# Kernel optimization log

Measured on AMD Instinct MI355X. Metric: run time of the kernel, lower is better.

## Reference

```python
import jax, jax.numpy as jnp
import numpy as np

D_MODEL = 1024
N_HEADS = 16
HEAD_DIM = D_MODEL // N_HEADS
D_FF = 4096
ROPE_RANK = 16
LN_EPS = 1e-5


def _ln(x, g, b):
    mu = jnp.mean(x, axis=-1, keepdims=True)
    var = jnp.mean((x - mu) ** 2, axis=-1, keepdims=True)
    return (x - mu) * jax.lax.rsqrt(var + LN_EPS) * g + b


def _rope(x, A, B_):
    # x: [B, T, D]; learned low-rank additive correction to sin/cos tables
    B, T, D = x.shape
    pos = jnp.arange(T, dtype=jnp.float32)
    theta = 1.0 / (10000.0 ** (jnp.arange(0, D, 2, dtype=jnp.float32) / D))  # [D/2]
    angles = pos[:, None] * theta[None, :]                                   # [T, D/2]
    sin_pos, cos_pos = jnp.sin(angles), jnp.cos(angles)
    base = jnp.concatenate([sin_pos, cos_pos], axis=-1)                      # [T, D]
    learned = (base @ A) @ B_                                                # [T, D]
    l_sin, l_cos = jnp.split(learned, 2, axis=-1)
    sin_f = sin_pos + l_sin                                                  # [T, D/2]
    cos_f = cos_pos + l_cos
    xe, xo = x[..., ::2], x[..., 1::2]
    re = xe * cos_f[None] - xo * sin_f[None]
    ro = xe * sin_f[None] + xo * cos_f[None]
    return jnp.stack([re, ro], axis=-1).reshape(B, T, D)


def setup_inputs() -> dict:
    key = jax.random.key(0)
    ks = jax.random.split(key, 20)
    B, T = 2, 2048
    s = 1.0 / np.sqrt(D_MODEL)
    sf = 1.0 / np.sqrt(D_FF)
    sr = 1.0 / np.sqrt(ROPE_RANK)
    return {
        "tgt": jax.random.normal(ks[0], (B, T, D_MODEL), jnp.float32),
        "Wq": jax.random.normal(ks[1], (D_MODEL, D_MODEL), jnp.float32) * s,
        "bq": jnp.zeros((D_MODEL,), jnp.float32),
        "Wk": jax.random.normal(ks[2], (D_MODEL, D_MODEL), jnp.float32) * s,
        "bk": jnp.zeros((D_MODEL,), jnp.float32),
        "Wv": jax.random.normal(ks[3], (D_MODEL, D_MODEL), jnp.float32) * s,
        "bv": jnp.zeros((D_MODEL,), jnp.float32),
        "Wo": jax.random.normal(ks[4], (D_MODEL, D_MODEL), jnp.float32) * s,
        "bo": jnp.zeros((D_MODEL,), jnp.float32),
        "W1": jax.random.normal(ks[5], (D_MODEL, D_FF), jnp.float32) * s,
        "b1": jnp.zeros((D_FF,), jnp.float32),
        "W2": jax.random.normal(ks[6], (D_FF, D_MODEL), jnp.float32) * sf,
        "b2": jnp.zeros((D_MODEL,), jnp.float32),
        "ln1_g": jnp.ones((D_MODEL,), jnp.float32),
        "ln1_b": jnp.zeros((D_MODEL,), jnp.float32),
        "ln2_g": jnp.ones((D_MODEL,), jnp.float32),
        "ln2_b": jnp.zeros((D_MODEL,), jnp.float32),
        "rope_A": jax.random.normal(ks[7], (D_MODEL, ROPE_RANK), jnp.float32) * s,
        "rope_B": jax.random.normal(ks[8], (ROPE_RANK, D_MODEL), jnp.float32) * sr,
    }


def reference(tgt, Wq, bq, Wk, bk, Wv, bv, Wo, bo, W1, b1, W2, b2,
              ln1_g, ln1_b, ln2_g, ln2_b, rope_A, rope_B):
    x = tgt
    B, T, D = x.shape
    q = _rope(x @ Wq + bq, rope_A, rope_B)
    k = _rope(x @ Wk + bk, rope_A, rope_B)
    v = x @ Wv + bv
    # [B, H, T, hd]
    q = q.reshape(B, T, N_HEADS, HEAD_DIM).transpose(0, 2, 1, 3)
    k = k.reshape(B, T, N_HEADS, HEAD_DIM).transpose(0, 2, 1, 3)
    v = v.reshape(B, T, N_HEADS, HEAD_DIM).transpose(0, 2, 1, 3)
    scores = jnp.einsum("bhqd,bhkd->bhqk", q, k) / np.sqrt(HEAD_DIM)
    attn = jax.nn.softmax(scores, axis=-1)  # no mask: module applies none
    ctx = jnp.einsum("bhqk,bhkd->bhqd", attn, v)
    ctx = ctx.transpose(0, 2, 1, 3).reshape(B, T, D)
    x = x + (ctx @ Wo + bo)
    x = _ln(x, ln1_g, ln1_b)
    ff = jax.nn.relu(x @ W1 + b1) @ W2 + b2
    x = _ln(x + ff, ln2_g, ln2_b)
    return x
```

## Files before the change

### kernel.cpp

```cpp
#include <hip/hip_runtime.h>
#include <math.h>

typedef unsigned short u16;
typedef unsigned int u32;
typedef __attribute__((ext_vector_type(8))) short short8v;
typedef __attribute__((ext_vector_type(4))) float f32x4;

__device__ __forceinline__ u16 f2bf(float f) {
    u32 u = __float_as_uint(f);
    u32 r = (u + 0x7fffu + ((u >> 16) & 1u)) >> 16;
    return (u16)r;
}

#define GLOAD_LDS(g, l)                                                        \
    __builtin_amdgcn_global_load_lds(                                          \
        (const __attribute__((address_space(1))) void*)(g),                    \
        (__attribute__((address_space(3))) void*)(l), 16, 0, 0)

__global__ void cast_k(const float* __restrict__ x, u16* __restrict__ y) {
    const int gid = blockIdx.x * blockDim.x + threadIdx.x;
    float4 v = ((const float4*)x)[gid];
    ushort4 o;
    o.x = f2bf(v.x); o.y = f2bf(v.y); o.z = f2bf(v.z); o.w = f2bf(v.w);
    ((ushort4*)y)[gid] = o;
}

__global__ __launch_bounds__(256) void tcast_k(const float* __restrict__ S,
                                               u16* __restrict__ Dt,
                                               int K, int N) {
    __shared__ float tile[32][33];
    const int n0 = blockIdx.x * 32, k0 = blockIdx.y * 32;
    const int tx = threadIdx.x & 31, ty = threadIdx.x >> 5;
#pragma unroll
    for (int i = 0; i < 4; i++)
        tile[ty + 8 * i][tx] = S[(size_t)(k0 + ty + 8 * i) * N + n0 + tx];
    __syncthreads();
#pragma unroll
    for (int i = 0; i < 4; i++)
        Dt[(size_t)(n0 + ty + 8 * i) * K + k0 + tx] = f2bf(tile[tx][ty + 8 * i]);
}

__global__ __launch_bounds__(256) void vtrans_k(const u16* __restrict__ vv,
                                                u16* __restrict__ Vt) {
    __shared__ u16 tile[32][33];
    const int key0 = blockIdx.x * 32, d0 = blockIdx.y * 32, bh = blockIdx.z;
    const int b = bh >> 4, h = bh & 15;
    const int tx = threadIdx.x & 31, ty = threadIdx.x >> 5;
#pragma unroll
    for (int i = 0; i < 4; i++)
        tile[ty + 8 * i][tx] =
            vv[(size_t)(b * 2048 + key0 + ty + 8 * i) * 1024 + h * 64 + d0 + tx];
    __syncthreads();
#pragma unroll
    for (int i = 0; i < 4; i++) {
        const int d = d0 + ty + 8 * i;
        const int key = key0 + tx;
        const int ksw = (key & ~63) | ((((key >> 3) & 7) ^ (d & 7)) << 3) | (key & 7);
        Vt[((size_t)bh * 64 + d) * 2048 + ksw] = tile[tx][ty + 8 * i];
    }
}

#define ROPE_LOG2C (13.287712379549449f / 512.0f)

__global__ __launch_bounds__(256) void rope1_k(const float* __restrict__ A,
                                               float* __restrict__ P) {
    __shared__ float sc[16][17];
    __shared__ float cc[16][17];
    __shared__ float Als[16][17];
    __shared__ float Alc[16][17];
    const int tid = threadIdx.x;
    const int tt = tid >> 4, rr = tid & 15;
    const int t = blockIdx.x * 16 + tt;
    float acc = 0.f;
    for (int i0 = 0; i0 < 512; i0 += 16) {
        __syncthreads();
        {
            const int i = i0 + rr;
            const float th = exp2f(-(float)i * ROPE_LOG2C);
            const float ang = (float)t * th;
            sc[tt][rr] = sinf(ang);
            cc[tt][rr] = cosf(ang);
            Als[tt][rr] = A[(i0 + tt) * 16 + rr];
            Alc[tt][rr] = A[(512 + i0 + tt) * 16 + rr];
        }
        __syncthreads();
#pragma unroll
        for (int ii = 0; ii < 16; ++ii)
            acc = fmaf(sc[tt][ii], Als[ii][rr],
                       fmaf(cc[tt][ii], Alc[ii][rr], acc));
    }
    P[t * 16 + rr] = acc;
}

__global__ void rope2_k(const float* __restrict__ P, const float* __restrict__ Bw,
                        float* __restrict__ sf, float* __restrict__ cf) {
    const int gid = blockIdx.x * blockDim.x + threadIdx.x;
    if (gid >= 2048 * 512) return;
    const int t = gid >> 9, i = gid & 511;
    float ls = 0.f, lc = 0.f;
#pragma unroll
    for (int r = 0; r < 16; ++r) {
        const float p = P[t * 16 + r];
        ls = fmaf(p, Bw[r * 1024 + i], ls);
        lc = fmaf(p, Bw[r * 1024 + 512 + i], lc);
    }
    const float th = exp2f(-(float)i * ROPE_LOG2C);
    const float ang = (float)t * th;
    sf[gid] = sinf(ang) + ls;
    cf[gid] = cosf(ang) + lc;
}

__device__ __forceinline__ void xcd_tile(int L, int xn, int rn, int rm,
                                         int& tm, int& tn) {
    const int xcd = L & 7, i = L >> 3;
    const int cx = xcd % xn, cy = xcd / xn;
    tn = cx * rn + (i % rn);
    tm = cy * rm + (i / rn);
}

enum { EP_NONE = 0, EP_RES = 2, EP_RELU = 3 };

template <int EPI, bool CBF, int BN>
__global__ __launch_bounds__(256) void mgemm_k(
    const u16* __restrict__ A, const u16* __restrict__ Bt,
    const float* __restrict__ bias, const float* __restrict__ resf,
    void* __restrict__ Cp, int M, int N, int K, int xn, int rn, int rm) {
    constexpr int NT = BN / 32;
    __shared__ u16 As[2 * 128 * 32];
    __shared__ u16 Bs[2 * BN * 32];
    const int tid = threadIdx.x;
    const int w = tid >> 6, l = tid & 63;
    const int quad = l >> 4, lr = l & 15;
    const int wr = w >> 1, wc = w & 1;
    int tm, tn;
    xcd_tile(blockIdx.x, xn, rn, rm, tm, tn);
    const int m0 = tm * 128, n0 = tn * BN;

    const int srow = w * 16 + (l >> 2);
    const int scol = (l & 3) * 8;
    const u16* ag0 = A + (size_t)(m0 + srow) * K + scol;
    const u16* ag1 = A + (size_t)(m0 + 64 + srow) * K + scol;
    const u16* bg0 = Bt + (size_t)(n0 + srow) * K + scol;
    const u16* bg1 = Bt + (size_t)(n0 + 64 + srow) * K + scol;

    f32x4 acc[4][NT];
#pragma unroll
    for (int i = 0; i < 4; i++)
#pragma unroll
        for (int j = 0; j < NT; j++) acc[i][j] = (f32x4)(0.0f);

    {
        u16* Ab = As;
        u16* Bb = Bs;
        GLOAD_LDS(ag0, Ab + w * 512);
        GLOAD_LDS(ag1, Ab + 2048 + w * 512);
        GLOAD_LDS(bg0, Bb + w * 512);
        if (BN == 128) GLOAD_LDS(bg1, Bb + 2048 + w * 512);
    }

    const int niter = K >> 5;
    for (int i = 0; i < niter; ++i) {
        __syncthreads();
        const int knext = (i + 1) << 5;
        if (knext < K) {
            u16* Ab = As + ((i + 1) & 1) * 4096;
            u16* Bb = Bs + ((i + 1) & 1) * (BN * 32);
            GLOAD_LDS(ag0 + knext, Ab + w * 512);
            GLOAD_LDS(ag1 + knext, Ab + 2048 + w * 512);
            GLOAD_LDS(bg0 + knext, Bb + w * 512);
            if (BN == 128) GLOAD_LDS(bg1 + knext, Bb + 2048 + w * 512);
        }
        const u16* Ac = As + (i & 1) * 4096;
        const u16* Bc = Bs + (i & 1) * (BN * 32);
        short8v af[4], bf[NT];
#pragma unroll
        for (int mt = 0; mt < 4; ++mt)
            af[mt] = *(const short8v*)&Ac[(wr * 64 + mt * 16 + lr) * 32 + quad * 8];
#pragma unroll
        for (int nt = 0; nt < NT; ++nt)
            bf[nt] = *(const short8v*)&Bc[(wc * (BN / 2) + nt * 16 + lr) * 32 + quad * 8];
#pragma unroll
        for (int mt = 0; mt < 4; ++mt)
#pragma unroll
            for (int nt = 0; nt < NT; ++nt)
                acc[mt][nt] = __builtin_amdgcn_mfma_f32_16x16x32_bf16(
                    af[mt], bf[nt], acc[mt][nt], 0, 0, 0);
    }

#pragma unroll
    for (int mt = 0; mt < 4; ++mt) {
#pragma unroll
        for (int nt = 0; nt < NT; ++nt) {
            const int n = n0 + wc * (BN / 2) + nt * 16 + lr;
            const float bb = bias[n];
#pragma unroll
            for (int reg = 0; reg < 4; ++reg) {
                const int m = m0 + wr * 64 + mt * 16 + quad * 4 + reg;
                float v = acc[mt][nt][reg] + bb;
                if (EPI == EP_RES) v += resf[(size_t)m * N + n];
                if (EPI == EP_RELU) v = fmaxf(v, 0.f);
                if (CBF) ((u16*)Cp)[(size_t)m * N + n] = f2bf(v);
                else     ((float*)Cp)[(size_t)m * N + n] = v;
            }
        }
    }
}

__global__ __launch_bounds__(256) void mqkv_k(
    const u16* __restrict__ A, const u16* __restrict__ Bt,
    const float* __restrict__ bq, const float* __restrict__ bk,
    const float* __restrict__ bv, const float* __restrict__ sf,
    const float* __restrict__ cf, u16* __restrict__ out) {
    const int K = 1024;
    __shared__ u16 As[2 * 128 * 32];
    __shared__ u16 Bs[2 * 128 * 32];
    const int tid = threadIdx.x;
    const int w = tid >> 6, l = tid & 63;
    const int quad = l >> 4, lr = l & 15;
    const int wr = w >> 1, wc = w & 1;
    int tm, tn;
    xcd_tile(blockIdx.x, 4, 6, 16, tm, tn);
    const int m0 = tm * 128, n0 = tn * 128;

    const int srow = w * 16 + (l >> 2);
    const int scol = (l & 3) * 8;
    const u16* ag0 = A + (size_t)(m0 + srow) * K + scol;
    const u16* ag1 = A + (size_t)(m0 + 64 + srow) * K + scol;
    const u16* bg0 = Bt + (size_t)(n0 + srow) * K + scol;
    const u16* bg1 = Bt + (size_t)(n0 + 64 + srow) * K + scol;

    f32x4 acc[4][4];
#pragma unroll
    for (int i = 0; i < 4; i++)
#pragma unroll
        for (int j = 0; j < 4; j++) acc[i][j] = (f32x4)(0.0f);

    {
        GLOAD_LDS(ag0, As + w * 512);
        GLOAD_LDS(ag1, As + 2048 + w * 512);
        GLOAD_LDS(bg0, Bs + w * 512);
        GLOAD_LDS(bg1, Bs + 2048 + w * 512);
    }
    for (int i = 0; i < 32; ++i) {
        __syncthreads();
        const int knext = (i + 1) << 5;
        if (knext < K) {
            u16* Ab = As + ((i + 1) & 1) * 4096;
            u16* Bb = Bs + ((i + 1) & 1) * 4096;
            GLOAD_LDS(ag0 + knext, Ab + w * 512);
            GLOAD_LDS(ag1 + knext, Ab + 2048 + w * 512);
            GLOAD_LDS(bg0 + knext, Bb + w * 512);
            GLOAD_LDS(bg1 + knext, Bb + 2048 + w * 512);
        }
        const u16* Ac = As + (i & 1) * 4096;
        const u16* Bc = Bs + (i & 1) * 4096;
        short8v af[4], bf[4];
#pragma unroll
        for (int mt = 0; mt < 4; ++mt)
            af[mt] = *(const short8v*)&Ac[(wr * 64 + mt * 16 + lr) * 32 + quad * 8];
#pragma unroll
        for (int nt = 0; nt < 4; ++nt)
            bf[nt] = *(const short8v*)&Bc[(wc * 64 + nt * 16 + lr) * 32 + quad * 8];
#pragma unroll
        for (int mt = 0; mt < 4; ++mt)
#pragma unroll
            for (int nt = 0; nt < 4; ++nt)
                acc[mt][nt] = __builtin_amdgcn_mfma_f32_16x16x32_bf16(
                    af[mt], bf[nt], acc[mt][nt], 0, 0, 0);
    }

    const int which = n0 >> 10;
    const float* bias = which == 0 ? bq : (which == 1 ? bk : bv);
    const bool doRope = which < 2;
    u16* Cp = out + (size_t)which * 4096 * 1024;

#pragma unroll
    for (int mt = 0; mt < 4; ++mt) {
#pragma unroll
        for (int nt = 0; nt < 4; ++nt) {
            const int n = n0 + wc * 64 + nt * 16 + lr;
            const int col = n & 1023;
            const float bb = bias[col];
#pragma unroll
            for (int reg = 0; reg < 4; ++reg) {
                const int m = m0 + wr * 64 + mt * 16 + quad * 4 + reg;
                float v = acc[mt][nt][reg] + bb;
                const float partner = __shfl_xor(v, 1);
                int colw = col;
                if (doRope) {
                    const int t = m & 2047;
                    const int fi = col >> 1;
                    const float svv = sf[t * 512 + fi];
                    const float cvv = cf[t * 512 + fi];
                    v = (col & 1) ? fmaf(partner, svv, v * cvv)
                                  : fmaf(v, cvv, -partner * svv);
                    if (which == 0) v *= 0.125f;
                    colw = (col & ~63) | ((((col >> 3) & 7) ^ (m & 7)) << 3) |
                           (col & 7);
                }
                Cp[(size_t)m * 1024 + colw] = f2bf(v);
            }
        }
    }
}

__global__ __launch_bounds__(256) void mattn_k(
    const u16* __restrict__ Q, const u16* __restrict__ Kg,
    const u16* __restrict__ Vt, u16* __restrict__ O) {
    __shared__ u16 Qs[64 * 64];
    __shared__ u16 Ks[64 * 64];
    __shared__ u16 Vs[64 * 64];
    __shared__ u16 Ps[4][16][72];
    const int tid = threadIdx.x;
    const int w = tid >> 6, l = tid & 63;
    const int quad = l >> 4, lr = l & 15;
    const int L = blockIdx.x;
    const int bh = (L & 7) * 4 + ((L >> 3) & 3);
    const int b = bh >> 4, h = bh & 15;
    const int row0 = (L >> 5) * 64;
    const size_t base = (size_t)b * 2048 * 1024 + (size_t)h * 64;
    const size_t vbase = (size_t)bh * 64 * 2048;

    const int dr = l >> 3;
    const int dc = (l & 7) * 8;
    const int g0 = w * 2, g1 = w * 2 + 1;

    GLOAD_LDS(Q + base + (size_t)(row0 + g0 * 8 + dr) * 1024 + dc, Qs + g0 * 512);
    GLOAD_LDS(Q + base + (size_t)(row0 + g1 * 8 + dr) * 1024 + dc, Qs + g1 * 512);
    __syncthreads();
    const int qr = w * 16 + lr;
    const short8v aq0 = *(const short8v*)&Qs[qr * 64 + ((quad ^ (qr & 7)) << 3)];
    const short8v aq1 = *(const short8v*)&Qs[qr * 64 + (((quad + 4) ^ (qr & 7)) << 3)];

    float lsum[4] = {0.f, 0.f, 0.f, 0.f};
    f32x4 o_acc[4];
#pragma unroll
    for (int nt = 0; nt < 4; nt++) o_acc[nt] = (f32x4)(0.0f);

    for (int kc = 0; kc < 2048; kc += 64) {
        __syncthreads();
        GLOAD_LDS(Kg + base + (size_t)(kc + g0 * 8 + dr) * 1024 + dc, Ks + g0 * 512);
        GLOAD_LDS(Kg + base + (size_t)(kc + g1 * 8 + dr) * 1024 + dc, Ks + g1 * 512);
        GLOAD_LDS(Vt + vbase + (size_t)(g0 * 8 + dr) * 2048 + kc + dc, Vs + g0 * 512);
        GLOAD_LDS(Vt + vbase + (size_t)(g1 * 8 + dr) * 2048 + kc + dc, Vs + g1 * 512);
        __syncthreads();

        f32x4 s[4];
#pragma unroll
        for (int nt = 0; nt < 4; nt++) s[nt] = (f32x4)(0.0f);
#pragma unroll
        for (int nt = 0; nt < 4; nt++) {
            const int kr = nt * 16 + lr;
            short8v bk0 = *(const short8v*)&Ks[kr * 64 + ((quad ^ (kr & 7)) << 3)];
            short8v bk1 = *(const short8v*)&Ks[kr * 64 + (((quad + 4) ^ (kr & 7)) << 3)];
            s[nt] = __builtin_amdgcn_mfma_f32_16x16x32_bf16(aq0, bk0, s[nt], 0, 0, 0);
            s[nt] = __builtin_amdgcn_mfma_f32_16x16x32_bf16(aq1, bk1, s[nt], 0, 0, 0);
        }

#pragma unroll
        for (int nt = 0; nt < 4; nt++) {
#pragma unroll
            for (int reg = 0; reg < 4; reg++) {
                const float p = __expf(s[nt][reg]);
                lsum[reg] += p;
                Ps[w][quad * 4 + reg][nt * 16 + lr] = f2bf(p);
            }
        }
        const short8v ap0 = *(const short8v*)&Ps[w][lr][quad * 8];
        const short8v ap1 = *(const short8v*)&Ps[w][lr][32 + quad * 8];
#pragma unroll
        for (int nt = 0; nt < 4; nt++) {
            const int vr = nt * 16 + lr;
            short8v vf0 = *(const short8v*)&Vs[vr * 64 + ((quad ^ (vr & 7)) << 3)];
            short8v vf1 = *(const short8v*)&Vs[vr * 64 + (((quad + 4) ^ (vr & 7)) << 3)];
            o_acc[nt] = __builtin_amdgcn_mfma_f32_16x16x32_bf16(ap0, vf0, o_acc[nt], 0, 0, 0);
            o_acc[nt] = __builtin_amdgcn_mfma_f32_16x16x32_bf16(ap1, vf1, o_acc[nt], 0, 0, 0);
        }
    }

    float l_i[4];
#pragma unroll
    for (int reg = 0; reg < 4; reg++) {
        float t = lsum[reg];
        t += __shfl_xor(t, 1);
        t += __shfl_xor(t, 2);
        t += __shfl_xor(t, 4);
        t += __shfl_xor(t, 8);
        l_i[reg] = t;
    }

#pragma unroll
    for (int nt = 0; nt < 4; nt++)
#pragma unroll
        for (int reg = 0; reg < 4; reg++) {
            const float out = o_acc[nt][reg] / l_i[reg];
            O[base + (size_t)(row0 + w * 16 + quad * 4 + reg) * 1024 +
              nt * 16 + lr] = f2bf(out);
        }
}

__global__ __launch_bounds__(256) void ln_k(
    const float* __restrict__ X, const float* __restrict__ g,
    const float* __restrict__ bb, float* __restrict__ outf,
    u16* __restrict__ outb) {
    const int row = blockIdx.x, tid = threadIdx.x;
    const float* x = X + (size_t)row * 1024;
    float4 xv = *(const float4*)&x[tid * 4];
    float s = xv.x + xv.y + xv.z + xv.w;
    float s2 = xv.x * xv.x + xv.y * xv.y + xv.z * xv.z + xv.w * xv.w;
#pragma unroll
    for (int msk = 32; msk >= 1; msk >>= 1) {
        s += __shfl_xor(s, msk);
        s2 += __shfl_xor(s2, msk);
    }
    __shared__ float red[8];
    const int wv = tid >> 6;
    if ((tid & 63) == 0) { red[wv] = s; red[wv + 4] = s2; }
    __syncthreads();
    s = red[0] + red[1] + red[2] + red[3];
    s2 = red[4] + red[5] + red[6] + red[7];
    const float mu = s * (1.f / 1024.f);
    float var = s2 * (1.f / 1024.f) - mu * mu;
    var = fmaxf(var, 0.f);
    const float rstd = rsqrtf(var + 1e-5f);
    float4 g4 = *(const float4*)&g[tid * 4];
    float4 b4 = *(const float4*)&bb[tid * 4];
    float o0 = (xv.x - mu) * rstd * g4.x + b4.x;
    float o1 = (xv.y - mu) * rstd * g4.y + b4.y;
    float o2 = (xv.z - mu) * rstd * g4.z + b4.z;
    float o3 = (xv.w - mu) * rstd * g4.w + b4.w;
    if (outf)
        *(float4*)(outf + (size_t)row * 1024 + tid * 4) = make_float4(o0, o1, o2, o3);
    if (outb) {
        ushort4 ov;
        ov.x = f2bf(o0); ov.y = f2bf(o1); ov.z = f2bf(o2); ov.w = f2bf(o3);
        *(ushort4*)(outb + (size_t)row * 1024 + tid * 4) = ov;
    }
}

extern "C" void kernel_launch(void* const* d_in, const int* in_sizes, int n_in,
                              void* d_out, int out_size, void* d_ws, size_t ws_size,
                              hipStream_t stream) {
    const float* tgt = (const float*)d_in[0];
    const float* Wq  = (const float*)d_in[1];
    const float* bq  = (const float*)d_in[2];
    const float* Wk  = (const float*)d_in[3];
    const float* bk  = (const float*)d_in[4];
    const float* Wv  = (const float*)d_in[5];
    const float* bv  = (const float*)d_in[6];
    const float* Wo  = (const float*)d_in[7];
    const float* bo  = (const float*)d_in[8];
    const float* W1  = (const float*)d_in[9];
    const float* b1  = (const float*)d_in[10];
    const float* W2  = (const float*)d_in[11];
    const float* b2  = (const float*)d_in[12];
    const float* g1  = (const float*)d_in[13];
    const float* be1 = (const float*)d_in[14];
    const float* g2  = (const float*)d_in[15];
    const float* be2 = (const float*)d_in[16];
    const float* rA  = (const float*)d_in[17];
    const float* rB  = (const float*)d_in[18];

    const int M = 4096, D = 1024, DFF = 4096;
    const size_t MD = (size_t)M * D;
    const size_t MB = 1u << 20;
    char* wsb = (char*)d_ws;

    u16* q    = (u16*)wsb;
    u16* vv   = q + 2 * MD;
    u16* ctx  = q + 3 * MD;
    u16* h    = q;
    float* x1  = (float*)(wsb + 32 * MB);
    float* sfp = (float*)(wsb + 48 * MB);
    float* cfp = sfp + (size_t)2048 * 512;
    u16* x1b  = (u16*)sfp;
    u16* tgtb = (u16*)(wsb + 56 * MB);
    u16* Vt   = (u16*)(wsb + 56 * MB);
    u16* Wqt  = (u16*)(wsb + 64 * MB);
    u16* Wkt  = (u16*)(wsb + 66 * MB);
    u16* Wvt  = (u16*)(wsb + 68 * MB);
    u16* Wot  = (u16*)(wsb + 70 * MB);
    u16* W1t  = (u16*)(wsb + 72 * MB);
    u16* W2t  = (u16*)(wsb + 80 * MB);
    float* Pp = (float*)(wsb + 88 * MB);

    cast_k<<<dim3(4096), dim3(256), 0, stream>>>(tgt, tgtb);
    tcast_k<<<dim3(32, 32),  dim3(256), 0, stream>>>(Wq, Wqt, D, D);
    tcast_k<<<dim3(32, 32),  dim3(256), 0, stream>>>(Wk, Wkt, D, D);
    tcast_k<<<dim3(32, 32),  dim3(256), 0, stream>>>(Wv, Wvt, D, D);
    tcast_k<<<dim3(32, 32),  dim3(256), 0, stream>>>(Wo, Wot, D, D);
    tcast_k<<<dim3(128, 32), dim3(256), 0, stream>>>(W1, W1t, D, DFF);
    tcast_k<<<dim3(32, 128), dim3(256), 0, stream>>>(W2, W2t, DFF, D);
    rope1_k<<<dim3(128), dim3(256), 0, stream>>>(rA, Pp);
    rope2_k<<<dim3(4096), dim3(256), 0, stream>>>(Pp, rB, sfp, cfp);

    mqkv_k<<<dim3(768), dim3(256), 0, stream>>>(
        tgtb, Wqt, bq, bk, bv, sfp, cfp, q);

    vtrans_k<<<dim3(64, 2, 32), dim3(256), 0, stream>>>(vv, Vt);

    mattn_k<<<dim3(1024), dim3(256), 0, stream>>>(q, q + MD, Vt, ctx);

    mgemm_k<EP_RES, false, 64><<<dim3(512), dim3(256), 0, stream>>>(
        ctx, Wot, bo, tgt, x1, M, D, D, 2, 8, 8);
    ln_k<<<dim3(4096), dim3(256), 0, stream>>>(x1, g1, be1, x1, x1b);
    mgemm_k<EP_RELU, true, 128><<<dim3(1024), dim3(256), 0, stream>>>(
        x1b, W1t, b1, nullptr, h, M, DFF, D, 4, 8, 16);
    mgemm_k<EP_RES, false, 64><<<dim3(512), dim3(256), 0, stream>>>(
        h, W2t, b2, x1, x1, M, D, DFF, 2, 8, 8);
    ln_k<<<dim3(4096), dim3(256), 0, stream>>>(x1, g2, be2, (float*)d_out, nullptr);

    (void)in_sizes; (void)n_in; (void)out_size; (void)ws_size;
}
```

Measured before the change: 471.8 us.

## Double-buffer K/V and widen attention tile to 128 query rows

Rewrites the attention kernel so each block handles 128 query rows (32 per wave), halving the grid and reusing each K/V tile across twice as many queries. K/V tiles are double-buffered so the next tile's global-to-LDS load overlaps the current compute, and one barrier per iteration replaces two. QK^T is computed transposed (K as A operand) so P can be written back into the Q LDS buffer with packed bf16 conversion, and launch bounds request 3 blocks per CU. The risk is higher register pressure from doubled accumulators and fewer blocks (512) to fill the GPU.

```diff
diff --git a/kernel.cpp b/kernel.cpp
--- a/kernel.cpp
+++ b/kernel.cpp
@@ -304,99 +304,159 @@
     }
 }
 
-__global__ __launch_bounds__(256) void mattn_k(
+__global__ __launch_bounds__(256, 3) void mattn_k(
     const u16* __restrict__ Q, const u16* __restrict__ Kg,
     const u16* __restrict__ Vt, u16* __restrict__ O) {
-    __shared__ u16 Qs[64 * 64];
-    __shared__ u16 Ks[64 * 64];
-    __shared__ u16 Vs[64 * 64];
-    __shared__ u16 Ps[4][16][72];
+    __shared__ u16 QPs[128 * 64];
+    __shared__ u16 Ks[2][64 * 64];
+    __shared__ u16 Vs[2][64 * 64];
     const int tid = threadIdx.x;
     const int w = tid >> 6, l = tid & 63;
     const int quad = l >> 4, lr = l & 15;
     const int L = blockIdx.x;
     const int bh = (L & 7) * 4 + ((L >> 3) & 3);
     const int b = bh >> 4, h = bh & 15;
-    const int row0 = (L >> 5) * 64;
+    const int row0 = (L >> 5) * 128;
     const size_t base = (size_t)b * 2048 * 1024 + (size_t)h * 64;
     const size_t vbase = (size_t)bh * 64 * 2048;
 
     const int dr = l >> 3;
     const int dc = (l & 7) * 8;
-    const int g0 = w * 2, g1 = w * 2 + 1;
-
-    GLOAD_LDS(Q + base + (size_t)(row0 + g0 * 8 + dr) * 1024 + dc, Qs + g0 * 512);
-    GLOAD_LDS(Q + base + (size_t)(row0 + g1 * 8 + dr) * 1024 + dc, Qs + g1 * 512);
+    const int g0 = w * 2, g1 = g0 + 1;
+    const u16* kg0 = Kg + base + (size_t)(g0 * 8 + dr) * 1024 + dc;
+    const u16* kg1 = Kg + base + (size_t)(g1 * 8 + dr) * 1024 + dc;
+    const u16* vg0 = Vt + vbase + (size_t)(g0 * 8 + dr) * 2048 + dc;
+    const u16* vg1 = Vt + vbase + (size_t)(g1 * 8 + dr) * 2048 + dc;
+
+#pragma unroll
+    for (int j = 0; j < 4; ++j) {
+        const int g = w * 4 + j;
+        GLOAD_LDS(Q + base + (size_t)(row0 + g * 8 + dr) * 1024 + dc,
+                  QPs + g * 512);
+    }
+    GLOAD_LDS(kg0, Ks[0] + g0 * 512);
+    GLOAD_LDS(kg1, Ks[0] + g1 * 512);
+    GLOAD_LDS(vg0, Vs[0] + g0 * 512);
+    GLOAD_LDS(vg1, Vs[0] + g1 * 512);
     __syncthreads();
-    const int qr = w * 16 + lr;
-    const short8v aq0 = *(const short8v*)&Qs[qr * 64 + ((quad ^ (qr & 7)) << 3)];
-    const short8v aq1 = *(const short8v*)&Qs[qr * 64 + (((quad + 4) ^ (qr & 7)) << 3)];
-
-    float lsum[4] = {0.f, 0.f, 0.f, 0.f};
-    f32x4 o_acc[4];
-#pragma unroll
-    for (int nt = 0; nt < 4; nt++) o_acc[nt] = (f32x4)(0.0f);
-
-    for (int kc = 0; kc < 2048; kc += 64) {
+
+    const int rsw = lr & 7;
+    short8v qf[2][2];
+#pragma unroll
+    for (int ntq = 0; ntq < 2; ++ntq) {
+        const int qr = w * 32 + ntq * 16 + lr;
+#pragma unroll
+        for (int kh = 0; kh < 2; ++kh)
+            qf[ntq][kh] = *(const short8v*)&QPs[qr * 64 +
+                (((kh * 4 + quad) ^ rsw) << 3)];
+    }
+
+    f32x4 o_acc[2][4];
+#pragma unroll
+    for (int i = 0; i < 2; ++i)
+#pragma unroll
+        for (int j = 0; j < 4; ++j) o_acc[i][j] = (f32x4)(0.0f);
+    float lsum[2] = {0.f, 0.f};
+
+    for (int i = 0; i < 32; ++i) {
         __syncthreads();
-        GLOAD_LDS(Kg + base + (size_t)(kc + g0 * 8 + dr) * 1024 + dc, Ks + g0 * 512);
-        GLOAD_LDS(Kg + base + (size_t)(kc + g1 * 8 + dr) * 1024 + dc, Ks + g1 * 512);
-        GLOAD_LDS(Vt + vbase + (size_t)(g0 * 8 + dr) * 2048 + kc + dc, Vs + g0 * 512);
-        GLOAD_LDS(Vt + vbase + (size_t)(g1 * 8 + dr) * 2048 + kc + dc, Vs + g1 * 512);
-        __syncthreads();
-
-        f32x4 s[4];
-#pragma unroll
-        for (int nt = 0; nt < 4; nt++) s[nt] = (f32x4)(0.0f);
-#pragma unroll
-        for (int nt = 0; nt < 4; nt++) {
-            const int kr = nt * 16 + lr;
-            short8v bk0 = *(const short8v*)&Ks[kr * 64 + ((quad ^ (kr & 7)) << 3)];
-            short8v bk1 = *(const short8v*)&Ks[kr * 64 + (((quad + 4) ^ (kr & 7)) << 3)];
-            s[nt] = __builtin_amdgcn_mfma_f32_16x16x32_bf16(aq0, bk0, s[nt], 0, 0, 0);
-            s[nt] = __builtin_amdgcn_mfma_f32_16x16x32_bf16(aq1, bk1, s[nt], 0, 0, 0);
-        }
-
-#pragma unroll
-        for (int nt = 0; nt < 4; nt++) {
-#pragma unroll
-            for (int reg = 0; reg < 4; reg++) {
-                const float p = __expf(s[nt][reg]);
-                lsum[reg] += p;
-                Ps[w][quad * 4 + reg][nt * 16 + lr] = f2bf(p);
+        if (i + 1 < 32) {
+            const size_t kro = (size_t)((i + 1) << 6) * 1024;
+            const int kco = (i + 1) << 6;
+            u16* Kb = Ks[(i + 1) & 1];
+            u16* Vb = Vs[(i + 1) & 1];
+            GLOAD_LDS(kg0 + kro, Kb + g0 * 512);
+            GLOAD_LDS(kg1 + kro, Kb + g1 * 512);
+            GLOAD_LDS(vg0 + kco, Vb + g0 * 512);
+            GLOAD_LDS(vg1 + kco, Vb + g1 * 512);
+        }
+        const u16* Kc = Ks[i & 1];
+        const u16* Vc = Vs[i & 1];
+
+        f32x4 s[4][2];
+#pragma unroll
+        for (int mt = 0; mt < 4; ++mt)
+#pragma unroll
+            for (int ntq = 0; ntq < 2; ++ntq) s[mt][ntq] = (f32x4)(0.0f);
+#pragma unroll
+        for (int mt = 0; mt < 4; ++mt) {
+            const int kr = mt * 16 + lr;
+            const short8v kf0 = *(const short8v*)&Kc[kr * 64 + ((quad ^ rsw) << 3)];
+            const short8v kf1 = *(const short8v*)&Kc[kr * 64 + (((quad + 4) ^ rsw) << 3)];
+#pragma unroll
+            for (int ntq = 0; ntq < 2; ++ntq) {
+                s[mt][ntq] = __builtin_amdgcn_mfma_f32_16x16x32_bf16(
+                    kf0, qf[ntq][0], s[mt][ntq], 0, 0, 0);
+                s[mt][ntq] = __builtin_amdgcn_mfma_f32_16x16x32_bf16(
+                    kf1, qf[ntq][1], s[mt][ntq], 0, 0, 0);
             }
         }
-        const short8v ap0 = *(const short8v*)&Ps[w][lr][quad * 8];
-        const short8v ap1 = *(const short8v*)&Ps[w][lr][32 + quad * 8];
-#pragma unroll
-        for (int nt = 0; nt < 4; nt++) {
-            const int vr = nt * 16 + lr;
-            short8v vf0 = *(const short8v*)&Vs[vr * 64 + ((quad ^ (vr & 7)) << 3)];
-            short8v vf1 = *(const short8v*)&Vs[vr * 64 + (((quad + 4) ^ (vr & 7)) << 3)];
-            o_acc[nt] = __builtin_amdgcn_mfma_f32_16x16x32_bf16(ap0, vf0, o_acc[nt], 0, 0, 0);
-            o_acc[nt] = __builtin_amdgcn_mfma_f32_16x16x32_bf16(ap1, vf1, o_acc[nt], 0, 0, 0);
-        }
-    }
-
-    float l_i[4];
-#pragma unroll
-    for (int reg = 0; reg < 4; reg++) {
-        float t = lsum[reg];
-        t += __shfl_xor(t, 1);
-        t += __shfl_xor(t, 2);
-        t += __shfl_xor(t, 4);
-        t += __shfl_xor(t, 8);
-        l_i[reg] = t;
-    }
-
-#pragma unroll
-    for (int nt = 0; nt < 4; nt++)
-#pragma unroll
-        for (int reg = 0; reg < 4; reg++) {
-            const float out = o_acc[nt][reg] / l_i[reg];
-            O[base + (size_t)(row0 + w * 16 + quad * 4 + reg) * 1024 +
-              nt * 16 + lr] = f2bf(out);
-        }
+
+#pragma unroll
+        for (int ntq = 0; ntq < 2; ++ntq) {
+            const int prow = w * 32 + ntq * 16 + lr;
+#pragma unroll
+            for (int mt = 0; mt < 4; ++mt) {
+                const float e0 = __expf(s[mt][ntq][0]);
+                const float e1 = __expf(s[mt][ntq][1]);
+                const float e2 = __expf(s[mt][ntq][2]);
+                const float e3 = __expf(s[mt][ntq][3]);
+                lsum[ntq] += (e0 + e1) + (e2 + e3);
+                u32 p01, p23;
+                asm("v_cvt_pk_bf16_f32 %0, %1, %2" : "=v"(p01) : "v"(e0), "v"(e1));
+                asm("v_cvt_pk_bf16_f32 %0, %1, %2" : "=v"(p23) : "v"(e2), "v"(e3));
+                uint2 pv; pv.x = p01; pv.y = p23;
+                *(uint2*)&QPs[prow * 64 +
+                              (((mt * 2 + (quad >> 1)) ^ rsw) << 3) +
+                              (quad & 1) * 4] = pv;
+            }
+        }
+
+        short8v vf[4][2];
+#pragma unroll
+        for (int ntd = 0; ntd < 4; ++ntd) {
+            const int vr = ntd * 16 + lr;
+            vf[ntd][0] = *(const short8v*)&Vc[vr * 64 + ((quad ^ rsw) << 3)];
+            vf[ntd][1] = *(const short8v*)&Vc[vr * 64 + (((quad + 4) ^ rsw) << 3)];
+        }
+        short8v pf[2][2];
+#pragma unroll
+        for (int mtq = 0; mtq < 2; ++mtq) {
+            const int prow = w * 32 + mtq * 16 + lr;
+            pf[mtq][0] = *(const short8v*)&QPs[prow * 64 + ((quad ^ rsw) << 3)];
+            pf[mtq][1] = *(const short8v*)&QPs[prow * 64 + (((quad + 4) ^ rsw) << 3)];
+        }
+#pragma unroll
+        for (int mtq = 0; mtq < 2; ++mtq)
+#pragma unroll
+            for (int ntd = 0; ntd < 4; ++ntd) {
+                o_acc[mtq][ntd] = __builtin_amdgcn_mfma_f32_16x16x32_bf16(
+                    pf[mtq][0], vf[ntd][0], o_acc[mtq][ntd], 0, 0, 0);
+                o_acc[mtq][ntd] = __builtin_amdgcn_mfma_f32_16x16x32_bf16(
+                    pf[mtq][1], vf[ntd][1], o_acc[mtq][ntd], 0, 0, 0);
+            }
+    }
+
+    float rden[2];
+#pragma unroll
+    for (int ntq = 0; ntq < 2; ++ntq) {
+        float t = lsum[ntq];
+        t += __shfl_xor(t, 16);
+        t += __shfl_xor(t, 32);
+        rden[ntq] = 1.0f / t;
+    }
+#pragma unroll
+    for (int mtq = 0; mtq < 2; ++mtq) {
+#pragma unroll
+        for (int reg = 0; reg < 4; ++reg) {
+            const float dsc = __shfl(rden[mtq], quad * 4 + reg);
+            const int m = row0 + w * 32 + mtq * 16 + quad * 4 + reg;
+#pragma unroll
+            for (int ntd = 0; ntd < 4; ++ntd)
+                O[base + (size_t)m * 1024 + ntd * 16 + lr] =
+                    f2bf(o_acc[mtq][ntd][reg] * dsc);
+        }
+    }
 }
 
 __global__ __launch_bounds__(256) void ln_k(
@@ -499,7 +559,7 @@
 
     vtrans_k<<<dim3(64, 2, 32), dim3(256), 0, stream>>>(vv, Vt);
 
-    mattn_k<<<dim3(1024), dim3(256), 0, stream>>>(q, q + MD, Vt, ctx);
+    mattn_k<<<dim3(512), dim3(256), 0, stream>>>(q, q + MD, Vt, ctx);
 
     mgemm_k<EP_RES, false, 64><<<dim3(512), dim3(256), 0, stream>>>(
         ctx, Wot, bo, tgt, x1, M, D, D, 2, 8, 8);
```

Result: faster. 459.4 us (-2.6%).
